# Kernel tuning notes

Measured on AMD Instinct MI355X. Metric: run time of the kernel, lower is better.

Reference implementation:

```python
import jax, jax.numpy as jnp
import numpy as np

K = 3          # involution kernel size
GROUPS = 32    # channels == GROUPS * K*K
BN_EPS = 1e-5

def _conv1x1(x, W, b):
    # x: (B,C,H,W), W: (Co,C), b: (Co,)
    return jnp.einsum('bchw,oc->bohw', x, W) + b[None, :, None, None]

def setup_inputs() -> dict:
    key = jax.random.key(0)
    ks = jax.random.split(key, 5)
    C = GROUPS * K * K  # 288
    x = jax.random.normal(ks[0], (8, C, 64, 64), dtype=jnp.float32)
    Wi = jax.random.normal(ks[1], (C, C), dtype=jnp.float32) * 0.05
    bi = jnp.zeros((C,), dtype=jnp.float32)
    gamma = jnp.ones((C,), dtype=jnp.float32)
    beta = jnp.zeros((C,), dtype=jnp.float32)
    Wo = jax.random.normal(ks[2], (C, C), dtype=jnp.float32) * 0.05
    bo = jnp.zeros((C,), dtype=jnp.float32)
    return {"x": x, "Wi": Wi, "bi": bi, "gamma": gamma, "beta": beta, "Wo": Wo, "bo": bo}

def reference(x, Wi, bi, gamma, beta, Wo, bo):
    B, C, H, W = x.shape
    # kernel generation branch (stride=1 -> avgpool is identity)
    tmp = jax.nn.relu(_conv1x1(x, Wi, bi))
    # BatchNorm2d in training mode: batch stats over (N,H,W), biased variance
    mean = jnp.mean(tmp, axis=(0, 2, 3), keepdims=True)
    var = jnp.var(tmp, axis=(0, 2, 3), keepdims=True)
    tmp = (tmp - mean) * jax.lax.rsqrt(var + BN_EPS)
    tmp = tmp * gamma[None, :, None, None] + beta[None, :, None, None]
    ker = _conv1x1(tmp, Wo, bo)                       # (B, G*K^2, H, W)
    ker = ker.reshape(B, GROUPS, K * K, H, W)         # (B, G, K^2, H, W)
    # unfold: extract KxK patches with padding (K-1)//2, stride 1
    p = (K - 1) // 2
    xp = jnp.pad(x, ((0, 0), (0, 0), (p, p), (p, p)))
    patches = jnp.stack(
        [xp[:, :, i:i + H, j:j + W] for i in range(K) for j in range(K)],
        axis=2,
    )  # (B, C, K^2, H, W), kernel-position minor — matches torch unfold layout
    patches = patches.reshape(B, GROUPS, C // GROUPS, K * K, H, W)
    # per-pixel dynamic kernel multiply + sum over kernel positions
    out = jnp.einsum('bgkhw,bgckhw->bgchw', ker, patches)
    return out.reshape(B, C, H, W)
```

## Files before the change

kernel.cpp:

```cpp
#include <hip/hip_runtime.h>

#define CH   288
#define GRPS 32
#define CPG  9
#define IMH  64
#define IMW  64
#define HW   4096
#define NB   8
#define NPX  (NB * HW)
#define BN_EPS 1e-5f
#define NSLOT 64

typedef short bf16x8 __attribute__((ext_vector_type(8)));
typedef float f32x4  __attribute__((ext_vector_type(4)));

#define XT_OFF   0u
#define WIB_OFF  18874368u
#define WOS_OFF  19040256u
#define SC_OFF   19208448u
#define SH_OFF   19209600u
#define BO2_OFF  19210752u


__device__ __forceinline__ unsigned short f2b(float f) {
    unsigned int u = __float_as_uint(f);
    return (unsigned short)((u + 0x7fffu + ((u >> 16) & 1u)) >> 16);
}
__device__ __forceinline__ float b2f(unsigned short h) {
    return __uint_as_float(((unsigned int)h) << 16);
}

#define GLDS(g, l) __builtin_amdgcn_global_load_lds( \
    (const __attribute__((address_space(1))) void*)(g), \
    (__attribute__((address_space(3))) void*)(l), 16, 0, 0)

__device__ __forceinline__ f32x4 mfma16(bf16x8 a, bf16x8 b, f32x4 c) {
    return __builtin_amdgcn_mfma_f32_16x16x32_bf16(a, b, c, 0, 0, 0);
}

#define STAGE_X32(XSRC) do {                                                   \
    for (int s = wave; s < 18; s += 4) {                                       \
        const int d   = s * 1024 + lane * 16;                                  \
        const int px  = d / 576;                                               \
        const int rem = d - px * 576;                                          \
        const int kc  = rem >> 6;                                              \
        const int ch  = (rem >> 4) & 3;                                        \
        const int sc  = ch ^ ((px >> 1) & 3);                                  \
        GLDS((XSRC) + (size_t)px * CH + kc * 32 + sc * 8, smc + s * 1024);     \
    }                                                                          \
} while (0)

#define TS 40
__global__ __launch_bounds__(256) void k_pre(const float* __restrict__ x,
                                             unsigned short* __restrict__ xt,
                                             const float* __restrict__ Wi,
                                             unsigned short* __restrict__ WibF,
                                             float* __restrict__ slots) {
    __shared__ unsigned short T[64 * TS];
    const int tid = threadIdx.x;
    const int p0 = blockIdx.x * 64;
    const int c0 = blockIdx.y * 32;
    const int b  = blockIdx.z;

    if (blockIdx.z == 0) {
        if (blockIdx.y == 0) {
            for (int i = blockIdx.x * 256 + tid; i < NSLOT * 576; i += 64 * 256)
                slots[i] = 0.0f;
        } else if (blockIdx.y == 1) {
            for (int id = blockIdx.x * 256 + tid; id < 162 * 64; id += 64 * 256) {
                const int t    = id >> 6;
                const int lane = id & 63;
                const int q    = lane >> 4;
                const int r    = lane & 15;
                const int jt   = t / 9;
                const int kk   = t - jt * 9;
                const int row  = jt * 16 + r;
                const int k0   = kk * 32 + q * 8;
                const float4 a = *(const float4*)(Wi + (size_t)row * CH + k0);
                const float4 bq = *(const float4*)(Wi + (size_t)row * CH + k0 + 4);
                unsigned short h[8] = {f2b(a.x), f2b(a.y), f2b(a.z), f2b(a.w),
                                       f2b(bq.x), f2b(bq.y), f2b(bq.z), f2b(bq.w)};
                *(uint4*)(WibF + (size_t)t * 512 + lane * 8) = *(const uint4*)h;
            }
        }
    }

    #pragma unroll
    for (int it = 0; it < 2; ++it) {
        const int item  = it * 256 + tid;
        const int c_loc = item >> 4;
        const int p4    = item & 15;
        const float4 v = *(const float4*)(x + (size_t)(b * CH + c0 + c_loc) * HW + p0 + p4 * 4);
        const int px = p4 * 4;
        T[(px + 0) * TS + c_loc] = f2b(v.x);
        T[(px + 1) * TS + c_loc] = f2b(v.y);
        T[(px + 2) * TS + c_loc] = f2b(v.z);
        T[(px + 3) * TS + c_loc] = f2b(v.w);
    }
    __syncthreads();
    const int px_loc = tid >> 2;
    const int cq     = tid & 3;
    const uint4 o = *(const uint4*)((const char*)T + px_loc * (TS * 2) + cq * 16);
    *(uint4*)(xt + ((size_t)b * HW + p0 + px_loc) * CH + c0 + cq * 8) = o;
}

__global__ __launch_bounds__(256) void k_gemm1(const unsigned short* __restrict__ WibF,
                                               const float* __restrict__ bi,
                                               unsigned short* __restrict__ xt,
                                               float* __restrict__ slots) {
    __shared__ char smc[20736];

    const int tid  = threadIdx.x;
    const int wave = tid >> 6;
    const int lane = tid & 63;
    const int q    = lane >> 4;
    const int r    = lane & 15;
    const int pxh  = wave & 1;
    const int chh  = wave >> 1;
    const int p0   = blockIdx.x * 32;

    f32x4 acc[9];
    #pragma unroll
    for (int j = 0; j < 9; ++j) acc[j] = (f32x4)0.0f;

    STAGE_X32(xt + (size_t)p0 * CH);
    asm volatile("s_waitcnt vmcnt(0)" ::: "memory");
    __syncthreads();

    #pragma unroll
    for (int kk = 0; kk < 9; ++kk) {
        const int xr = pxh * 16 + r;
        const bf16x8 xf = *(const bf16x8*)(smc + xr * 576 + kk * 64 +
                                           ((q ^ ((xr >> 1) & 3)) * 16));
        #pragma unroll
        for (int j = 0; j < 9; ++j) {
            const bf16x8 wf = *(const bf16x8*)(WibF +
                (size_t)((chh * 9 + j) * 9 + kk) * 512 + lane * 8);
            acc[j] = mfma16(wf, xf, acc[j]);
        }
    }
    __syncthreads();

    float* sstat = (float*)(smc + 18432);
    for (int c2 = tid; c2 < 576; c2 += 256) sstat[c2] = 0.0f;
    __syncthreads();

    #pragma unroll 1
    for (int j = 0; j < 9; ++j) {
        const int cb = chh * 144 + j * 16 + q * 4;
        const float4 b4 = *(const float4*)(bi + cb);
        float v[4];
        v[0] = fmaxf(acc[j][0] + b4.x, 0.0f);
        v[1] = fmaxf(acc[j][1] + b4.y, 0.0f);
        v[2] = fmaxf(acc[j][2] + b4.z, 0.0f);
        v[3] = fmaxf(acc[j][3] + b4.w, 0.0f);
        unsigned short h[4] = {f2b(v[0]), f2b(v[1]), f2b(v[2]), f2b(v[3])};
        *(uint2*)(smc + (pxh * 16 + r) * 576 + cb * 2) = *(const uint2*)h;
        float a1[4] = {v[0], v[1], v[2], v[3]};
        float a2[4] = {v[0]*v[0], v[1]*v[1], v[2]*v[2], v[3]*v[3]};
        #pragma unroll
        for (int m = 1; m < 16; m <<= 1) {
            #pragma unroll
            for (int i = 0; i < 4; ++i) {
                a1[i] += __shfl_xor(a1[i], m, 64);
                a2[i] += __shfl_xor(a2[i], m, 64);
            }
        }
        if (r == 0) {
            #pragma unroll
            for (int i = 0; i < 4; ++i) {
                atomicAdd(&sstat[cb + i], a1[i]);
                atomicAdd(&sstat[288 + cb + i], a2[i]);
            }
        }
    }
    __syncthreads();

    for (int idx = tid; idx < 1152; idx += 256) {
        const int row = idx / 36;
        const int off = idx - row * 36;
        *(uint4*)(xt + (size_t)(p0 + row) * CH + off * 8) =
            *(const uint4*)(smc + row * 576 + off * 16);
    }
    float* slot = slots + (size_t)(blockIdx.x & (NSLOT - 1)) * 576;
    for (int c2 = tid; c2 < 576; c2 += 256)
        atomicAdd(&slot[c2], sstat[c2]);
}

__global__ __launch_bounds__(576) void k_scale(const float* __restrict__ slots,
                                               const float* __restrict__ gamma,
                                               const float* __restrict__ beta,
                                               float* __restrict__ scale,
                                               float* __restrict__ shift) {
    __shared__ float red[576];
    const int tid = threadIdx.x;
    float s = 0.0f;
    #pragma unroll 4
    for (int sl = 0; sl < NSLOT; ++sl) s += slots[sl * 576 + tid];
    red[tid] = s;
    __syncthreads();
    if (tid < CH) {
        const float inv  = 1.0f / (float)(NB * HW);
        const float mean = red[tid] * inv;
        const float var  = red[288 + tid] * inv - mean * mean;
        const float rs   = rsqrtf(var + BN_EPS);
        const float sc   = gamma[tid] * rs;
        scale[tid] = sc;
        shift[tid] = beta[tid] - mean * sc;
    }
}

__global__ __launch_bounds__(64) void k_fold(const float* __restrict__ Wo,
                                             const float* __restrict__ bo,
                                             const float* __restrict__ scale,
                                             const float* __restrict__ shift,
                                             unsigned short* __restrict__ WosF,
                                             float* __restrict__ bo2) {
    const int m = blockIdx.x;
    const int t = threadIdx.x;
    float s = 0.0f;
    for (int k = t; k < CH; k += 64) s += Wo[(size_t)m * CH + k] * shift[k];
    #pragma unroll
    for (int off = 32; off > 0; off >>= 1) s += __shfl_down(s, off, 64);
    if (t == 0) bo2[m] = bo[m] + s;

    if (t < 36) {
        const int kk = t >> 2;
        const int q  = t & 3;
        const int jt = m >> 4;
        const int rr = m & 15;
        const int k0 = kk * 32 + q * 8;
        unsigned short h[8];
        #pragma unroll
        for (int j = 0; j < 8; ++j)
            h[j] = f2b(Wo[(size_t)m * CH + k0 + j] * scale[k0 + j]);
        *(uint4*)(WosF + (size_t)(jt * 9 + kk) * 512 + (q * 16 + rr) * 8) =
            *(const uint4*)h;
    }
}

#define KLS 36
__global__ __launch_bounds__(256) void k_gemm2_invol(const unsigned short* __restrict__ xt,
                                                     const unsigned short* __restrict__ WosF,
                                                     const float* __restrict__ bo2,
                                                     const float* __restrict__ x,
                                                     float* __restrict__ out) {
    __shared__ char smc[20736];
    unsigned short* kerL = (unsigned short*)smc;

    const int tid  = threadIdx.x;
    const int wave = tid >> 6;
    const int lane = tid & 63;
    const int q    = lane >> 4;
    const int r    = lane & 15;
    const int pxh  = wave & 1;
    const int chh  = wave >> 1;
    const int p0   = blockIdx.x * 32;
    const int b    = blockIdx.y;
    const int h    = p0 >> 6;
    const int w0   = p0 & 63;
    const size_t rowbase = (size_t)b * HW + p0;

    f32x4 acc[9];
    #pragma unroll
    for (int j = 0; j < 9; ++j) acc[j] = (f32x4)0.0f;

    STAGE_X32(xt + rowbase * CH);
    asm volatile("s_waitcnt vmcnt(0)" ::: "memory");
    __syncthreads();

    #pragma unroll
    for (int kk = 0; kk < 9; ++kk) {
        const int xr = pxh * 16 + r;
        const bf16x8 xf = *(const bf16x8*)(smc + xr * 576 + kk * 64 +
                                           ((q ^ ((xr >> 1) & 3)) * 16));
        #pragma unroll
        for (int j = 0; j < 9; ++j) {
            const bf16x8 wf = *(const bf16x8*)(WosF +
                (size_t)((chh * 9 + j) * 9 + kk) * 512 + lane * 8);
            acc[j] = mfma16(wf, xf, acc[j]);
        }
    }
    __syncthreads();

    const int pxl = pxh * 16 + r;
    #pragma unroll
    for (int j = 0; j < 9; ++j) {
        const int cb = chh * 144 + j * 16 + q * 4;
        const float4 bz = *(const float4*)(bo2 + cb);
        kerL[(cb + 0) * KLS + pxl] = f2b(acc[j][0] + bz.x);
        kerL[(cb + 1) * KLS + pxl] = f2b(acc[j][1] + bz.y);
        kerL[(cb + 2) * KLS + pxl] = f2b(acc[j][2] + bz.z);
        kerL[(cb + 3) * KLS + pxl] = f2b(acc[j][3] + bz.w);
    }
    __syncthreads();

    const int tm = tid >> 3;
    const int tn = tid & 7;
    const int wb = w0 + tn * 4;
    #pragma unroll 1
    for (int i = 0; i < 9; ++i) {
        const int ch = tm + 32 * i;
        const int cb = (ch / CPG) * CPG;
        float xv[3][6];
        #pragma unroll
        for (int dr = 0; dr < 3; ++dr) {
            const int hh = h + dr - 1;
            const bool rv = (hh >= 0) && (hh < IMH);
            const float* xr2 = x + ((size_t)(b * CH + ch) * IMH + (rv ? hh : 0)) * IMW;
            if (rv) {
                const float4 m4 = *(const float4*)(xr2 + wb);
                xv[dr][1] = m4.x; xv[dr][2] = m4.y; xv[dr][3] = m4.z; xv[dr][4] = m4.w;
                xv[dr][0] = (wb > 0)       ? xr2[wb - 1] : 0.0f;
                xv[dr][5] = (wb + 4 < IMW) ? xr2[wb + 4] : 0.0f;
            } else {
                #pragma unroll
                for (int j = 0; j < 6; ++j) xv[dr][j] = 0.0f;
            }
        }
        float o[4] = {0.0f, 0.0f, 0.0f, 0.0f};
        #pragma unroll
        for (int k = 0; k < 9; ++k) {
            const int dr = k / 3, dc = k % 3;
            const uint2 kk = *(const uint2*)(kerL + (cb + k) * KLS + tn * 4);
            const unsigned short* ks = (const unsigned short*)&kk;
            #pragma unroll
            for (int j = 0; j < 4; ++j)
                o[j] += b2f(ks[j]) * xv[dr][j + dc];
        }
        float4 ov = {o[0], o[1], o[2], o[3]};
        *(float4*)(out + ((size_t)(b * CH + ch) * IMH + h) * IMW + wb) = ov;
    }
}

extern "C" void kernel_launch(void* const* d_in, const int* in_sizes, int n_in,
                              void* d_out, int out_size, void* d_ws, size_t ws_size,
                              hipStream_t stream) {
    const float* x     = (const float*)d_in[0];
    const float* Wi    = (const float*)d_in[1];
    const float* bi    = (const float*)d_in[2];
    const float* gamma = (const float*)d_in[3];
    const float* beta  = (const float*)d_in[4];
    const float* Wo    = (const float*)d_in[5];
    const float* bo    = (const float*)d_in[6];
    float* out = (float*)d_out;

    char* ws = (char*)d_ws;
    unsigned short* xt   = (unsigned short*)(ws + XT_OFF);
    unsigned short* WibF = (unsigned short*)(ws + WIB_OFF);
    unsigned short* WosF = (unsigned short*)(ws + WOS_OFF);
    float* slots = (float*)(ws + WOS_OFF);
    float* scale = (float*)(ws + SC_OFF);
    float* shift = (float*)(ws + SH_OFF);
    float* bo2   = (float*)(ws + BO2_OFF);

    k_pre<<<dim3(HW / 64, CH / 32, NB), 256, 0, stream>>>(x, xt, Wi, WibF, slots);
    k_gemm1<<<dim3(NPX / 32), 256, 0, stream>>>(WibF, bi, xt, slots);
    k_scale<<<dim3(1), 576, 0, stream>>>(slots, gamma, beta, scale, shift);
    k_fold<<<dim3(CH), 64, 0, stream>>>(Wo, bo, scale, shift, WosF, bo2);
    k_gemm2_invol<<<dim3(HW / 32, NB), 256, 0, stream>>>(xt, WosF, bo2, x, out);
}
```

Measured before the change: 198.6 us.

## Fuse x transpose/convert into first GEMM and swizzle second GEMM block order

Removes the separate pre-pass that transposed x to pixel-major bf16. The first GEMM now stages fp32 x tiles directly into LDS in channel-major order and converts them to bf16 fragments on the fly. This drops a full read-write round trip of the activation tensor, at the cost of a larger LDS footprint and strided, possibly bank-conflicting LDS reads plus conversion work inside the GEMM. Weight conversion and slot zeroing move to a small kernel, and the second kernel's block index is remapped to interleave batches.

Result: faster. 190.3 us (-4.2%).

```diff
diff --git a/kernel.cpp b/kernel.cpp
--- a/kernel.cpp
+++ b/kernel.cpp
@@ -14,7 +14,7 @@
 typedef short bf16x8 __attribute__((ext_vector_type(8)));
 typedef float f32x4  __attribute__((ext_vector_type(4)));
 
-#define XT_OFF   0u
+#define TMP_OFF  0u
 #define WIB_OFF  18874368u
 #define WOS_OFF  19040256u
 #define SC_OFF   19208448u
@@ -50,65 +50,34 @@
     }                                                                          \
 } while (0)
 
-#define TS 40
-__global__ __launch_bounds__(256) void k_pre(const float* __restrict__ x,
-                                             unsigned short* __restrict__ xt,
-                                             const float* __restrict__ Wi,
+__global__ __launch_bounds__(256) void k_cvt(const float* __restrict__ Wi,
                                              unsigned short* __restrict__ WibF,
                                              float* __restrict__ slots) {
-    __shared__ unsigned short T[64 * TS];
-    const int tid = threadIdx.x;
-    const int p0 = blockIdx.x * 64;
-    const int c0 = blockIdx.y * 32;
-    const int b  = blockIdx.z;
-
-    if (blockIdx.z == 0) {
-        if (blockIdx.y == 0) {
-            for (int i = blockIdx.x * 256 + tid; i < NSLOT * 576; i += 64 * 256)
-                slots[i] = 0.0f;
-        } else if (blockIdx.y == 1) {
-            for (int id = blockIdx.x * 256 + tid; id < 162 * 64; id += 64 * 256) {
-                const int t    = id >> 6;
-                const int lane = id & 63;
-                const int q    = lane >> 4;
-                const int r    = lane & 15;
-                const int jt   = t / 9;
-                const int kk   = t - jt * 9;
-                const int row  = jt * 16 + r;
-                const int k0   = kk * 32 + q * 8;
-                const float4 a = *(const float4*)(Wi + (size_t)row * CH + k0);
-                const float4 bq = *(const float4*)(Wi + (size_t)row * CH + k0 + 4);
-                unsigned short h[8] = {f2b(a.x), f2b(a.y), f2b(a.z), f2b(a.w),
-                                       f2b(bq.x), f2b(bq.y), f2b(bq.z), f2b(bq.w)};
-                *(uint4*)(WibF + (size_t)t * 512 + lane * 8) = *(const uint4*)h;
-            }
-        }
-    }
-
-    #pragma unroll
-    for (int it = 0; it < 2; ++it) {
-        const int item  = it * 256 + tid;
-        const int c_loc = item >> 4;
-        const int p4    = item & 15;
-        const float4 v = *(const float4*)(x + (size_t)(b * CH + c0 + c_loc) * HW + p0 + p4 * 4);
-        const int px = p4 * 4;
-        T[(px + 0) * TS + c_loc] = f2b(v.x);
-        T[(px + 1) * TS + c_loc] = f2b(v.y);
-        T[(px + 2) * TS + c_loc] = f2b(v.z);
-        T[(px + 3) * TS + c_loc] = f2b(v.w);
-    }
-    __syncthreads();
-    const int px_loc = tid >> 2;
-    const int cq     = tid & 3;
-    const uint4 o = *(const uint4*)((const char*)T + px_loc * (TS * 2) + cq * 16);
-    *(uint4*)(xt + ((size_t)b * HW + p0 + px_loc) * CH + c0 + cq * 8) = o;
+    const int id = blockIdx.x * 256 + threadIdx.x;
+    if (id < 162 * 64) {
+        const int t    = id >> 6;
+        const int lane = id & 63;
+        const int q    = lane >> 4;
+        const int r    = lane & 15;
+        const int jt   = t / 9;
+        const int kk   = t - jt * 9;
+        const int row  = jt * 16 + r;
+        const int k0   = kk * 32 + q * 8;
+        const float4 a  = *(const float4*)(Wi + (size_t)row * CH + k0);
+        const float4 bq = *(const float4*)(Wi + (size_t)row * CH + k0 + 4);
+        unsigned short h[8] = {f2b(a.x), f2b(a.y), f2b(a.z), f2b(a.w),
+                               f2b(bq.x), f2b(bq.y), f2b(bq.z), f2b(bq.w)};
+        *(uint4*)(WibF + (size_t)t * 512 + lane * 8) = *(const uint4*)h;
+    }
+    for (int i = id; i < NSLOT * 576; i += 64 * 256) slots[i] = 0.0f;
 }
 
 __global__ __launch_bounds__(256) void k_gemm1(const unsigned short* __restrict__ WibF,
                                                const float* __restrict__ bi,
-                                               unsigned short* __restrict__ xt,
+                                               const float* __restrict__ x,
+                                               unsigned short* __restrict__ tmp,
                                                float* __restrict__ slots) {
-    __shared__ char smc[20736];
+    __shared__ char smc[36864];
 
     const int tid  = threadIdx.x;
     const int wave = tid >> 6;
@@ -118,20 +87,30 @@
     const int pxh  = wave & 1;
     const int chh  = wave >> 1;
     const int p0   = blockIdx.x * 32;
+    const int b    = p0 >> 12;
+    const int pi   = p0 & 4095;
 
     f32x4 acc[9];
     #pragma unroll
     for (int j = 0; j < 9; ++j) acc[j] = (f32x4)0.0f;
 
-    STAGE_X32(xt + (size_t)p0 * CH);
+    for (int s = wave; s < 36; s += 4) {
+        const int ch  = s * 8 + (lane >> 3);
+        const int pxo = (lane & 7) * 4;
+        GLDS(x + (size_t)(b * CH + ch) * HW + pi + pxo, smc + s * 1024);
+    }
     asm volatile("s_waitcnt vmcnt(0)" ::: "memory");
     __syncthreads();
 
+    const float* xl = (const float*)smc;
     #pragma unroll
     for (int kk = 0; kk < 9; ++kk) {
-        const int xr = pxh * 16 + r;
-        const bf16x8 xf = *(const bf16x8*)(smc + xr * 576 + kk * 64 +
-                                           ((q ^ ((xr >> 1) & 3)) * 16));
+        const int px = pxh * 16 + r;
+        unsigned short hh[8];
+        #pragma unroll
+        for (int j = 0; j < 8; ++j)
+            hh[j] = f2b(xl[(kk * 32 + q * 8 + j) * 32 + px]);
+        const bf16x8 xf = *(const bf16x8*)hh;
         #pragma unroll
         for (int j = 0; j < 9; ++j) {
             const bf16x8 wf = *(const bf16x8*)(WibF +
@@ -179,7 +158,7 @@
     for (int idx = tid; idx < 1152; idx += 256) {
         const int row = idx / 36;
         const int off = idx - row * 36;
-        *(uint4*)(xt + (size_t)(p0 + row) * CH + off * 8) =
+        *(uint4*)(tmp + (size_t)(p0 + row) * CH + off * 8) =
             *(const uint4*)(smc + row * 576 + off * 16);
     }
     float* slot = slots + (size_t)(blockIdx.x & (NSLOT - 1)) * 576;
@@ -240,7 +219,7 @@
 }
 
 #define KLS 36
-__global__ __launch_bounds__(256) void k_gemm2_invol(const unsigned short* __restrict__ xt,
+__global__ __launch_bounds__(256) void k_gemm2_invol(const unsigned short* __restrict__ tmp,
                                                      const unsigned short* __restrict__ WosF,
                                                      const float* __restrict__ bo2,
                                                      const float* __restrict__ x,
@@ -255,17 +234,20 @@
     const int r    = lane & 15;
     const int pxh  = wave & 1;
     const int chh  = wave >> 1;
-    const int p0   = blockIdx.x * 32;
-    const int b    = blockIdx.y;
-    const int h    = p0 >> 6;
-    const int w0   = p0 & 63;
+
+    const int bid = blockIdx.x;
+    const int sw  = (bid & 7) * 128 + (bid >> 3);
+    const int b   = sw >> 7;
+    const int p0  = (sw & 127) * 32;
+    const int h   = p0 >> 6;
+    const int w0  = p0 & 63;
     const size_t rowbase = (size_t)b * HW + p0;
 
     f32x4 acc[9];
     #pragma unroll
     for (int j = 0; j < 9; ++j) acc[j] = (f32x4)0.0f;
 
-    STAGE_X32(xt + rowbase * CH);
+    STAGE_X32(tmp + rowbase * CH);
     asm volatile("s_waitcnt vmcnt(0)" ::: "memory");
     __syncthreads();
 
@@ -346,7 +328,7 @@
     float* out = (float*)d_out;
 
     char* ws = (char*)d_ws;
-    unsigned short* xt   = (unsigned short*)(ws + XT_OFF);
+    unsigned short* tmp  = (unsigned short*)(ws + TMP_OFF);
     unsigned short* WibF = (unsigned short*)(ws + WIB_OFF);
     unsigned short* WosF = (unsigned short*)(ws + WOS_OFF);
     float* slots = (float*)(ws + WOS_OFF);
@@ -354,9 +336,9 @@
     float* shift = (float*)(ws + SH_OFF);
     float* bo2   = (float*)(ws + BO2_OFF);
 
-    k_pre<<<dim3(HW / 64, CH / 32, NB), 256, 0, stream>>>(x, xt, Wi, WibF, slots);
-    k_gemm1<<<dim3(NPX / 32), 256, 0, stream>>>(WibF, bi, xt, slots);
+    k_cvt<<<dim3(64), 256, 0, stream>>>(Wi, WibF, slots);
+    k_gemm1<<<dim3(NPX / 32), 256, 0, stream>>>(WibF, bi, x, tmp, slots);
     k_scale<<<dim3(1), 576, 0, stream>>>(slots, gamma, beta, scale, shift);
     k_fold<<<dim3(CH), 64, 0, stream>>>(Wo, bo, scale, shift, WosF, bo2);
-    k_gemm2_invol<<<dim3(HW / 32, NB), 256, 0, stream>>>(xt, WosF, bo2, x, out);
-}
+    k_gemm2_invol<<<dim3(NPX / 32), 256, 0, stream>>>(tmp, WosF, bo2, x, out);
+}
```
